# Kernel tuning notes

Measured on AMD Instinct MI355X. Metric: run time of the kernel, lower is better.

The kernel has to match this reference:

```python
import jax, jax.numpy as jnp
import numpy as np

LATENT = 1024

def setup_inputs() -> dict:
    key = jax.random.key(0)
    k1, k2, k3, k4 = jax.random.split(key, 4)
    B, T, D = 64, 512, LATENT
    h_t = jax.random.normal(k1, (B, D), dtype=jnp.float32)
    z = jax.random.normal(k2, (B, T, D), dtype=jnp.float32)
    # nn.Linear(2D, D): weight [D, 2D], bias [D]
    bound = 1.0 / np.sqrt(2 * D)
    W = jax.random.uniform(k3, (D, 2 * D), minval=-bound, maxval=bound, dtype=jnp.float32)
    b = jax.random.uniform(k4, (D,), minval=-bound, maxval=bound, dtype=jnp.float32)
    alpha = jnp.full((D,), 0.1, dtype=jnp.float32)
    return {"h_t": h_t, "z": z, "W": W, "b": b, "alpha": alpha}

def reference(h_t, z, W, b, alpha):
    # Split gate weight into h-part and z-part (concat([h,z]) @ W.T == h@Wh.T + z@Wz.T)
    D = h_t.shape[-1]
    Wh = W[:, :D]  # [D, D]
    Wz = W[:, D:]  # [D, D]
    leak = 1.0 - alpha  # [D]

    def step(h, z_t):
        gate = jax.nn.sigmoid(h @ Wh.T + z_t @ Wz.T + b)
        h_new = jnp.tanh(h * leak + gate * z_t)
        return h_new, h_new

    # scan over time: z is [B, T, D] -> [T, B, D]
    _, hs = jax.lax.scan(step, h_t, jnp.swapaxes(z, 0, 1))
    return jnp.swapaxes(hs, 0, 1)  # [B, T, D]
```

## Files before the change

### kernel.cpp

```cpp
#include <hip/hip_runtime.h>
#include <math.h>


#define D_ 1024
#define B_ 64
#define T_ 512

typedef _Float16 f16;
typedef _Float16 f16x8 __attribute__((ext_vector_type(8)));
typedef _Float16 f16x4 __attribute__((ext_vector_type(4)));
typedef float f32x4 __attribute__((ext_vector_type(4)));
typedef unsigned long long u64;

#define WS_WH16  0L
#define WS_WZ16  2097152L
#define WS_SLOTS 4194304L

__device__ __forceinline__ void gload_lds16(const void* g, void* l) {
  __builtin_amdgcn_global_load_lds(
      (const __attribute__((address_space(1))) void*)(g),
      (__attribute__((address_space(3))) void*)(l), 16, 0, 0);
}

__global__ __launch_bounds__(256) void k_prep(
    const float* __restrict__ W, const float* __restrict__ h0,
    f16* __restrict__ wh16, f16* __restrict__ wz16, u64* __restrict__ slots) {
  const int tid = blockIdx.x * 256 + threadIdx.x;
  {
    const long e = (long)tid * 4;
    const long j = e >> 11, c = e & 2047;
    float4 v = *(const float4*)(W + e);
    f16x4 o = {(f16)v.x, (f16)v.y, (f16)v.z, (f16)v.w};
    f16* dst = (c < D_) ? (wh16 + j * D_ + c) : (wz16 + j * D_ + (c - D_));
    *(f16x4*)dst = o;
  }
  if (tid < 65536) {
    if (tid < 32768) {
      const int b = tid >> 9, p = tid & 511;
      f16 fa = (f16)h0[(long)b * D_ + 2 * p];
      f16 fb = (f16)h0[(long)b * D_ + 2 * p + 1];
      unsigned u = (unsigned)*(unsigned short*)&fa |
                   ((unsigned)*(unsigned short*)&fb << 16);
      slots[tid] = (u64)u;
    } else {
      slots[tid] = 0xFFFFFFFF00000000ull;
    }
  }
}

__global__ __launch_bounds__(256) void k_gemm_zw(
    const float* __restrict__ zf, const f16* __restrict__ wz16,
    const float* __restrict__ bias, float* __restrict__ out) {
  __shared__ f16 ldsA[8 * 512];
  __shared__ f16 ldsB[8 * 512];
  const int tid = threadIdx.x, lane = tid & 63, w = tid >> 6;
  const int r16 = lane & 15, g8 = lane >> 4;
  const int nt = blockIdx.x & 7, mt = blockIdx.x >> 3;
  const long m0 = (long)mt * 128, n0 = (long)nt * 128;
  const int arow = tid >> 1, kh = (tid & 1) * 16;
  const float* gA = zf + (m0 + arow) * D_ + kh;
  const f16* gB = wz16 + (n0 + r16) * D_ + g8 * 8;
  const int wr = w >> 1, wc = w & 1;
  f32x4 acc[4][4] = {};
  float4 ra[4];
#pragma unroll
  for (int q = 0; q < 4; ++q) ra[q] = *(const float4*)(gA + q * 4);

  for (int ks = 0; ks < 32; ++ks) {
    if (ks) __syncthreads();
#pragma unroll
    for (int c = 0; c < 2; ++c) {
      const int ch = w * 2 + c;
      gload_lds16(gB + (long)ch * 16 * D_ + ks * 32, &ldsB[ch * 512]);
    }
    {
      const int ch = arow >> 4, lr = arow & 15;
#pragma unroll
      for (int hf = 0; hf < 2; ++hf) {
        float4 x = ra[hf * 2], y = ra[hf * 2 + 1];
        f16x8 v = {(f16)x.x, (f16)x.y, (f16)x.z, (f16)x.w,
                   (f16)y.x, (f16)y.y, (f16)y.z, (f16)y.w};
        const int kk = kh + hf * 8;
        *(f16x8*)(&ldsA[ch * 512 + (lr | ((kk >> 3) << 4)) * 8]) = v;
      }
    }
    __syncthreads();
    if (ks < 31) {
#pragma unroll
      for (int q = 0; q < 4; ++q)
        ra[q] = *(const float4*)(gA + (ks + 1) * 32 + q * 4);
    }
    f16x8 af[4], bf[4];
#pragma unroll
    for (int i = 0; i < 4; ++i)
      af[i] = *(const f16x8*)(&ldsA[(wr * 4 + i) * 512 + lane * 8]);
#pragma unroll
    for (int j = 0; j < 4; ++j)
      bf[j] = *(const f16x8*)(&ldsB[(wc * 4 + j) * 512 + lane * 8]);
#pragma unroll
    for (int i = 0; i < 4; ++i)
#pragma unroll
      for (int j = 0; j < 4; ++j)
        acc[i][j] = __builtin_amdgcn_mfma_f32_16x16x32_f16(af[i], bf[j], acc[i][j], 0, 0, 0);
  }

  float bj[4];
#pragma unroll
  for (int j = 0; j < 4; ++j) bj[j] = bias[n0 + wc * 64 + j * 16 + r16];
#pragma unroll
  for (int i = 0; i < 4; ++i) {
    const long mb = m0 + wr * 64 + i * 16 + g8 * 4;
#pragma unroll
    for (int j = 0; j < 4; ++j) {
      const long nn = n0 + wc * 64 + j * 16 + r16;
#pragma unroll
      for (int r = 0; r < 4; ++r)
        out[(mb + r) * D_ + nn] = acc[i][j][r] + bj[j];
    }
  }
}

__global__ __launch_bounds__(256, 1) void k_recur(
    const f16* __restrict__ wh16, u64* slots, const float* __restrict__ z,
    const float* __restrict__ h0, const float* __restrict__ alpha,
    float* __restrict__ out) {
  __shared__ char Hb[8192];
  __shared__ char Rd[2][5120];

  const int tid = threadIdx.x, lane = tid & 63, w = tid >> 6;
  const int bid = blockIdx.x;
  const int g = (bid & 7) * 2 + ((bid >> 3) & 1);
  const int rk = bid >> 4;
  const int j0 = rk * 64, b0 = g * 4;

  f16x8 bfr[32];
  {
    const f16* wb = wh16 + (long)(j0 + (lane & 15)) * D_ + w * 256 + (lane >> 4) * 8;
#pragma unroll
    for (int n = 0; n < 4; ++n)
#pragma unroll
      for (int kt = 0; kt < 8; ++kt)
        bfr[n * 8 + kt] = *(const f16x8*)(wb + (long)n * 16 * D_ + kt * 32);
  }

  const int jj = j0 + lane;
  const float lk = 1.0f - alpha[jj];
  float hp = h0[(long)(b0 + w) * D_ + jj];

  const int row = lane & 3, g8 = lane >> 4;

  for (int t = 0; t < T_; ++t) {
    const long off = ((long)(b0 + w) * T_ + t) * D_ + jj;
    float A = out[off];
    float Z = z[off];

    const u64* cur = slots + (long)(t & 1) * 32768 + (long)b0 * 512 + w * 128;
    u64 vv[8];
    unsigned pend = 0xFFu;
    for (int guard = 0; pend && guard < (1 << 18); ++guard) {
#pragma unroll
      for (int i = 0; i < 8; ++i)
        if (pend & (1u << i)) {
          const int idx = i * 64 + lane;
          vv[i] = __hip_atomic_load(cur + (idx >> 7) * 512 + (idx & 127),
                                    __ATOMIC_RELAXED, __HIP_MEMORY_SCOPE_AGENT);
        }
#pragma unroll
      for (int i = 0; i < 8; ++i)
        if ((pend & (1u << i)) && (unsigned)(vv[i] >> 32) == (unsigned)t)
          pend &= ~(1u << i);
    }

#pragma unroll
    for (int i = 0; i < 8; ++i) {
      const int idx = i * 64 + lane, b = idx >> 7, lp = idx & 127;
      *(unsigned*)(Hb + ((w * 2048 + b * 512 + lp * 4) ^ ((b & 1) << 6))) =
          (unsigned)vv[i];
    }

    f32x4 acc[4] = {{0,0,0,0},{0,0,0,0},{0,0,0,0},{0,0,0,0}};
#pragma unroll
    for (int kt = 0; kt < 8; ++kt) {
      f16x8 af = *(const f16x8*)(
          Hb + ((w * 2048 + row * 512 + kt * 64 + g8 * 16) ^ ((row & 1) << 6)));
#pragma unroll
      for (int n = 0; n < 4; ++n)
        acc[n] = __builtin_amdgcn_mfma_f32_16x16x32_f16(af, bfr[n * 8 + kt], acc[n], 0, 0, 0);
    }

    char* rd = Rd[t & 1];
#pragma unroll
    for (int n = 0; n < 4; ++n) {
      const f32x4 v = acc[n];
      const float val = (g8 & 1) ? ((g8 & 2) ? v[3] : v[1])
                                 : ((g8 & 2) ? v[2] : v[0]);
      *(float*)(rd + w * 1280 + g8 * 320 + n * 64 + (lane & 15) * 4) = val;
    }
    __syncthreads();

    float pre = 0.f;
#pragma unroll
    for (int kq = 0; kq < 4; ++kq)
      pre += *(const float*)(rd + kq * 1280 + w * 320 + lane * 4);

    const float gg = __builtin_amdgcn_rcpf(1.0f + __expf(-(pre + A)));
    float y = 2.0f * (hp * lk + gg * Z);
    y = fminf(fmaxf(y, -30.0f), 30.0f);
    const float ex = __expf(y);
    const float hn = (ex - 1.0f) * __builtin_amdgcn_rcpf(ex + 1.0f);
    hp = hn;

    const float q = __shfl_xor(hn, 1);
    if (!(lane & 1)) {
      f16 pa = (f16)hn, pb = (f16)q;
      const unsigned u = (unsigned)*(unsigned short*)&pa |
                         ((unsigned)*(unsigned short*)&pb << 16);
      const u64 val = (((u64)(unsigned)(t + 1)) << 32) | (u64)u;
      __hip_atomic_store(
          slots + (long)((t + 1) & 1) * 32768 + (long)(b0 + w) * 512 + (jj >> 1),
          val, __ATOMIC_RELAXED, __HIP_MEMORY_SCOPE_AGENT);
    }
    out[off] = hn;
  }
}

extern "C" void kernel_launch(void* const* d_in, const int* in_sizes, int n_in,
                              void* d_out, int out_size, void* d_ws, size_t ws_size,
                              hipStream_t stream) {
  const float* h_t = (const float*)d_in[0];
  const float* z = (const float*)d_in[1];
  const float* W = (const float*)d_in[2];
  const float* bias = (const float*)d_in[3];
  const float* alpha = (const float*)d_in[4];
  float* out = (float*)d_out;
  char* ws = (char*)d_ws;
  f16* wh16 = (f16*)(ws + WS_WH16);
  f16* wz16 = (f16*)(ws + WS_WZ16);
  u64* slots = (u64*)(ws + WS_SLOTS);

  k_prep<<<dim3(2048), dim3(256), 0, stream>>>(W, h_t, wh16, wz16, slots);
  k_gemm_zw<<<dim3(2048), dim3(256), 0, stream>>>(z, wz16, bias, out);
  k_recur<<<dim3(256), dim3(256), 0, stream>>>(wh16, slots, z, h_t, alpha, out);
}
```

Baseline: 1.360 ms.

## Fuse z@Wz GEMM into recurrent kernel, overlapping it with the spin-wait

New measurement: 1.458 ms. 7.3% more time.

```diff
diff --git a/kernel.cpp b/kernel.cpp
--- a/kernel.cpp
+++ b/kernel.cpp
@@ -15,12 +15,6 @@
 #define WS_WH16  0L
 #define WS_WZ16  2097152L
 #define WS_SLOTS 4194304L
-
-__device__ __forceinline__ void gload_lds16(const void* g, void* l) {
-  __builtin_amdgcn_global_load_lds(
-      (const __attribute__((address_space(1))) void*)(g),
-      (__attribute__((address_space(3))) void*)(l), 16, 0, 0);
-}
 
 __global__ __launch_bounds__(256) void k_prep(
     const float* __restrict__ W, const float* __restrict__ h0,
@@ -48,83 +42,13 @@
   }
 }
 
-__global__ __launch_bounds__(256) void k_gemm_zw(
-    const float* __restrict__ zf, const f16* __restrict__ wz16,
-    const float* __restrict__ bias, float* __restrict__ out) {
-  __shared__ f16 ldsA[8 * 512];
-  __shared__ f16 ldsB[8 * 512];
-  const int tid = threadIdx.x, lane = tid & 63, w = tid >> 6;
-  const int r16 = lane & 15, g8 = lane >> 4;
-  const int nt = blockIdx.x & 7, mt = blockIdx.x >> 3;
-  const long m0 = (long)mt * 128, n0 = (long)nt * 128;
-  const int arow = tid >> 1, kh = (tid & 1) * 16;
-  const float* gA = zf + (m0 + arow) * D_ + kh;
-  const f16* gB = wz16 + (n0 + r16) * D_ + g8 * 8;
-  const int wr = w >> 1, wc = w & 1;
-  f32x4 acc[4][4] = {};
-  float4 ra[4];
-#pragma unroll
-  for (int q = 0; q < 4; ++q) ra[q] = *(const float4*)(gA + q * 4);
-
-  for (int ks = 0; ks < 32; ++ks) {
-    if (ks) __syncthreads();
-#pragma unroll
-    for (int c = 0; c < 2; ++c) {
-      const int ch = w * 2 + c;
-      gload_lds16(gB + (long)ch * 16 * D_ + ks * 32, &ldsB[ch * 512]);
-    }
-    {
-      const int ch = arow >> 4, lr = arow & 15;
-#pragma unroll
-      for (int hf = 0; hf < 2; ++hf) {
-        float4 x = ra[hf * 2], y = ra[hf * 2 + 1];
-        f16x8 v = {(f16)x.x, (f16)x.y, (f16)x.z, (f16)x.w,
-                   (f16)y.x, (f16)y.y, (f16)y.z, (f16)y.w};
-        const int kk = kh + hf * 8;
-        *(f16x8*)(&ldsA[ch * 512 + (lr | ((kk >> 3) << 4)) * 8]) = v;
-      }
-    }
-    __syncthreads();
-    if (ks < 31) {
-#pragma unroll
-      for (int q = 0; q < 4; ++q)
-        ra[q] = *(const float4*)(gA + (ks + 1) * 32 + q * 4);
-    }
-    f16x8 af[4], bf[4];
-#pragma unroll
-    for (int i = 0; i < 4; ++i)
-      af[i] = *(const f16x8*)(&ldsA[(wr * 4 + i) * 512 + lane * 8]);
-#pragma unroll
-    for (int j = 0; j < 4; ++j)
-      bf[j] = *(const f16x8*)(&ldsB[(wc * 4 + j) * 512 + lane * 8]);
-#pragma unroll
-    for (int i = 0; i < 4; ++i)
-#pragma unroll
-      for (int j = 0; j < 4; ++j)
-        acc[i][j] = __builtin_amdgcn_mfma_f32_16x16x32_f16(af[i], bf[j], acc[i][j], 0, 0, 0);
-  }
-
-  float bj[4];
-#pragma unroll
-  for (int j = 0; j < 4; ++j) bj[j] = bias[n0 + wc * 64 + j * 16 + r16];
-#pragma unroll
-  for (int i = 0; i < 4; ++i) {
-    const long mb = m0 + wr * 64 + i * 16 + g8 * 4;
-#pragma unroll
-    for (int j = 0; j < 4; ++j) {
-      const long nn = n0 + wc * 64 + j * 16 + r16;
-#pragma unroll
-      for (int r = 0; r < 4; ++r)
-        out[(mb + r) * D_ + nn] = acc[i][j][r] + bj[j];
-    }
-  }
-}
-
 __global__ __launch_bounds__(256, 1) void k_recur(
-    const f16* __restrict__ wh16, u64* slots, const float* __restrict__ z,
-    const float* __restrict__ h0, const float* __restrict__ alpha,
+    const f16* __restrict__ wh16, const f16* __restrict__ wz16, u64* slots,
+    const float* __restrict__ z, const float* __restrict__ h0,
+    const float* __restrict__ alpha, const float* __restrict__ bias,
     float* __restrict__ out) {
   __shared__ char Hb[8192];
+  __shared__ char Hz[8192];
   __shared__ char Rd[2][5120];
 
   const int tid = threadIdx.x, lane = tid & 63, w = tid >> 6;
@@ -133,59 +57,93 @@
   const int rk = bid >> 4;
   const int j0 = rk * 64, b0 = g * 4;
 
-  f16x8 bfr[32];
+  f16x8 bfr[32], bfz[32];
   {
-    const f16* wb = wh16 + (long)(j0 + (lane & 15)) * D_ + w * 256 + (lane >> 4) * 8;
+    const long wo = (long)(j0 + (lane & 15)) * D_ + w * 256 + (lane >> 4) * 8;
+    const f16* wb = wh16 + wo;
+    const f16* wzb = wz16 + wo;
 #pragma unroll
     for (int n = 0; n < 4; ++n)
 #pragma unroll
-      for (int kt = 0; kt < 8; ++kt)
+      for (int kt = 0; kt < 8; ++kt) {
         bfr[n * 8 + kt] = *(const f16x8*)(wb + (long)n * 16 * D_ + kt * 32);
+        bfz[n * 8 + kt] = *(const f16x8*)(wzb + (long)n * 16 * D_ + kt * 32);
+      }
   }
 
   const int jj = j0 + lane;
   const float lk = 1.0f - alpha[jj];
+  const float bi = bias[jj];
   float hp = h0[(long)(b0 + w) * D_ + jj];
 
   const int row = lane & 3, g8 = lane >> 4;
 
+  float4 zreg[4];
+#pragma unroll
+  for (int cz = 0; cz < 4; ++cz)
+    zreg[cz] = *(const float4*)(z + ((long)(b0 + cz) * T_) * D_ + w * 256 + lane * 4);
+  float Z = z[((long)(b0 + w) * T_) * D_ + jj];
+
   for (int t = 0; t < T_; ++t) {
-    const long off = ((long)(b0 + w) * T_ + t) * D_ + jj;
-    float A = out[off];
-    float Z = z[off];
-
     const u64* cur = slots + (long)(t & 1) * 32768 + (long)b0 * 512 + w * 128;
     u64 vv[8];
-    unsigned pend = 0xFFu;
-    for (int guard = 0; pend && guard < (1 << 18); ++guard) {
-#pragma unroll
-      for (int i = 0; i < 8; ++i)
-        if (pend & (1u << i)) {
-          const int idx = i * 64 + lane;
-          vv[i] = __hip_atomic_load(cur + (idx >> 7) * 512 + (idx & 127),
-                                    __ATOMIC_RELAXED, __HIP_MEMORY_SCOPE_AGENT);
-        }
-#pragma unroll
-      for (int i = 0; i < 8; ++i)
-        if ((pend & (1u << i)) && (unsigned)(vv[i] >> 32) == (unsigned)t)
-          pend &= ~(1u << i);
-    }
-
 #pragma unroll
     for (int i = 0; i < 8; ++i) {
-      const int idx = i * 64 + lane, b = idx >> 7, lp = idx & 127;
-      *(unsigned*)(Hb + ((w * 2048 + b * 512 + lp * 4) ^ ((b & 1) << 6))) =
-          (unsigned)vv[i];
+      const int c = i >> 1, b = (lane >> 5) + 2 * (i & 1);
+      vv[i] = __hip_atomic_load(cur + b * 512 + c * 32 + (lane & 31),
+                                __ATOMIC_RELAXED, __HIP_MEMORY_SCOPE_AGENT);
+    }
+
+#pragma unroll
+    for (int cz = 0; cz < 4; ++cz) {
+      const float4 v = zreg[cz];
+      f16 pa = (f16)v.x, pb = (f16)v.y, pc = (f16)v.z, pd = (f16)v.w;
+      const unsigned lo = (unsigned)*(unsigned short*)&pa |
+                          ((unsigned)*(unsigned short*)&pb << 16);
+      const unsigned hi = (unsigned)*(unsigned short*)&pc |
+                          ((unsigned)*(unsigned short*)&pd << 16);
+      const u64 pv = (u64)lo | ((u64)hi << 32);
+      *(u64*)(Hz + ((w * 2048 + cz * 512 + lane * 8) ^ ((cz & 1) << 6))) = pv;
     }
 
     f32x4 acc[4] = {{0,0,0,0},{0,0,0,0},{0,0,0,0},{0,0,0,0}};
 #pragma unroll
     for (int kt = 0; kt < 8; ++kt) {
-      f16x8 af = *(const f16x8*)(
-          Hb + ((w * 2048 + row * 512 + kt * 64 + g8 * 16) ^ ((row & 1) << 6)));
+      f16x8 az = *(const f16x8*)(
+          Hz + ((w * 2048 + row * 512 + kt * 64 + g8 * 16) ^ ((row & 1) << 6)));
 #pragma unroll
       for (int n = 0; n < 4; ++n)
-        acc[n] = __builtin_amdgcn_mfma_f32_16x16x32_f16(af, bfr[n * 8 + kt], acc[n], 0, 0, 0);
+        acc[n] = __builtin_amdgcn_mfma_f32_16x16x32_f16(az, bfz[n * 8 + kt], acc[n], 0, 0, 0);
+    }
+
+#pragma unroll
+    for (int c = 0; c < 4; ++c) {
+      unsigned p2 = 3u;
+      for (int guard = 0; p2 && guard < (1 << 18); ++guard) {
+        if ((p2 & 1u) && (unsigned)(vv[2 * c] >> 32) == (unsigned)t) p2 &= ~1u;
+        if ((p2 & 2u) && (unsigned)(vv[2 * c + 1] >> 32) == (unsigned)t) p2 &= ~2u;
+        if (p2 & 1u)
+          vv[2 * c] = __hip_atomic_load(cur + ((lane >> 5) + 0) * 512 + c * 32 + (lane & 31),
+                                        __ATOMIC_RELAXED, __HIP_MEMORY_SCOPE_AGENT);
+        if (p2 & 2u)
+          vv[2 * c + 1] = __hip_atomic_load(cur + ((lane >> 5) + 2) * 512 + c * 32 + (lane & 31),
+                                            __ATOMIC_RELAXED, __HIP_MEMORY_SCOPE_AGENT);
+      }
+#pragma unroll
+      for (int i2 = 0; i2 < 2; ++i2) {
+        const int b = (lane >> 5) + 2 * i2;
+        *(unsigned*)(Hb + ((w * 2048 + b * 512 + (c * 32 + (lane & 31)) * 4) ^
+                           ((b & 1) << 6))) = (unsigned)vv[2 * c + i2];
+      }
+#pragma unroll
+      for (int k2 = 0; k2 < 2; ++k2) {
+        const int kt = 2 * c + k2;
+        f16x8 af = *(const f16x8*)(
+            Hb + ((w * 2048 + row * 512 + kt * 64 + g8 * 16) ^ ((row & 1) << 6)));
+#pragma unroll
+        for (int n = 0; n < 4; ++n)
+          acc[n] = __builtin_amdgcn_mfma_f32_16x16x32_f16(af, bfr[n * 8 + kt], acc[n], 0, 0, 0);
+      }
     }
 
     char* rd = Rd[t & 1];
@@ -198,12 +156,12 @@
     }
     __syncthreads();
 
-    float pre = 0.f;
+    float pre = bi;
 #pragma unroll
     for (int kq = 0; kq < 4; ++kq)
       pre += *(const float*)(rd + kq * 1280 + w * 320 + lane * 4);
 
-    const float gg = __builtin_amdgcn_rcpf(1.0f + __expf(-(pre + A)));
+    const float gg = __builtin_amdgcn_rcpf(1.0f + __expf(-pre));
     float y = 2.0f * (hp * lk + gg * Z);
     y = fminf(fmaxf(y, -30.0f), 30.0f);
     const float ex = __expf(y);
@@ -220,7 +178,16 @@
           slots + (long)((t + 1) & 1) * 32768 + (long)(b0 + w) * 512 + (jj >> 1),
           val, __ATOMIC_RELAXED, __HIP_MEMORY_SCOPE_AGENT);
     }
+
+    const int tn = (t + 1 < T_) ? t + 1 : t;
+#pragma unroll
+    for (int cz = 0; cz < 4; ++cz)
+      zreg[cz] = *(const float4*)(z + ((long)(b0 + cz) * T_ + tn) * D_ + w * 256 + lane * 4);
+    const long offn = ((long)(b0 + w) * T_ + tn) * D_ + jj;
+    const long off = ((long)(b0 + w) * T_ + t) * D_ + jj;
+    const float Znext = z[offn];
     out[off] = hn;
+    Z = Znext;
   }
 }
 
@@ -239,6 +206,5 @@
   u64* slots = (u64*)(ws + WS_SLOTS);
 
   k_prep<<<dim3(2048), dim3(256), 0, stream>>>(W, h_t, wh16, wz16, slots);
-  k_gemm_zw<<<dim3(2048), dim3(256), 0, stream>>>(z, wz16, bias, out);
-  k_recur<<<dim3(256), dim3(256), 0, stream>>>(wh16, slots, z, h_t, alpha, out);
+  k_recur<<<dim3(256), dim3(256), 0, stream>>>(wh16, wz16, slots, z, h_t, alpha, bias, out);
 }
```
